# Performance work log

Measured on AMD Instinct MI355X. Metric: run time of the kernel, lower is better.

Reference implementation:

```python
import jax, jax.numpy as jnp
import numpy as np

B, N, D = 8, 4096, 3

def setup_inputs() -> dict:
    key = jax.random.key(0)
    k1, k2 = jax.random.split(key)
    prediction = jax.random.normal(k1, (B, N, D), dtype=jnp.float32)
    ground_truth = jax.random.normal(k2, (B, N, D), dtype=jnp.float32)
    return {"prediction": prediction, "ground_truth": ground_truth}

def reference(prediction, ground_truth):
    batch_size, num, _ = prediction.shape
    # T[b, i, j] = ||pred[b, i] - gt[b, j]||^2  -> [B, N, N]
    diff = prediction[:, :, None, :] - ground_truth[:, None, :, :]
    T = jnp.sum(diff * diff, axis=-1)
    # squeeze() in torch is a no-op for B > 1
    cd_loss = jnp.sum(jnp.min(T, axis=1)) + jnp.sum(jnp.min(T, axis=2))
    return cd_loss / batch_size
```

## Files before the change

### kernel.cpp

```cpp
#include <hip/hip_runtime.h>

#define TPB 256
#define IPT 8
#define NIB 2
#define NPTS 4096
#define NB 8

typedef float v2f __attribute__((ext_vector_type(2)));

static __device__ __forceinline__ v2f pk_fma(v2f a, v2f b, v2f c) {
  v2f d;
  asm("v_pk_fma_f32 %0, %1, %2, %3" : "=v"(d) : "v"(a), "v"(b), "v"(c));
  return d;
}

__global__ __launch_bounds__(TPB, 4) void cd_partial_kernel(
    const float* __restrict__ pred, const float* __restrict__ gt,
    float* __restrict__ partial, float* __restrict__ out, int njb, int jchunk) {
  extern __shared__ float4 spr[];

  if (blockIdx.x == 0 && threadIdx.x == 0) *out = 0.0f;

  int bid = blockIdx.x;
  int jb  = bid % njb;  bid /= njb;
  int ib  = bid & (NIB - 1); bid /= NIB;
  int b   = bid & (NB - 1);  bid /= NB;
  int dir = bid;

  const float* src = (dir == 0) ? pred : gt;
  const float* tgt = (dir == 0) ? gt : pred;
  src += (size_t)b * NPTS * 3;
  tgt += (size_t)b * NPTS * 3;

  const int t = threadIdx.x;

  for (int j = t; j < jchunk; j += TPB) {
    int jj = jb * jchunk + j;
    float gx = tgt[jj * 3 + 0];
    float gy = tgt[jj * 3 + 1];
    float gz = tgt[jj * 3 + 2];
    float gw = fmaf(gx, gx, fmaf(gy, gy, gz * gz));
    int p = j >> 1, h = j & 1;
    float* base = (float*)&spr[2 * p];
    base[0 + h] = gx;
    base[2 + h] = gy;
    base[4 + h] = gz;
    base[6 + h] = gw;
  }

  const int ibase = ib * (TPB * IPT);
  const float4* sv = (const float4*)(src + (size_t)(ibase + t * IPT) * 3);
  float4 A = sv[0], B2 = sv[1], C = sv[2], D = sv[3], E = sv[4], F = sv[5];
  float x[IPT], y[IPT], z[IPT];
  x[0]=A.x;  y[0]=A.y;  z[0]=A.z;
  x[1]=A.w;  y[1]=B2.x; z[1]=B2.y;
  x[2]=B2.z; y[2]=B2.w; z[2]=C.x;
  x[3]=C.y;  y[3]=C.z;  z[3]=C.w;
  x[4]=D.x;  y[4]=D.y;  z[4]=D.z;
  x[5]=D.w;  y[5]=E.x;  z[5]=E.y;
  x[6]=E.z;  y[6]=E.w;  z[6]=F.x;
  x[7]=F.y;  y[7]=F.z;  z[7]=F.w;

  v2f qx2[IPT], qy2[IPT], qz2[IPT];
  float pp[IPT], mn[IPT];
#pragma unroll
  for (int k = 0; k < IPT; ++k) {
    float qx = -2.0f * x[k], qy = -2.0f * y[k], qz = -2.0f * z[k];
    qx2[k] = (v2f){qx, qx};
    qy2[k] = (v2f){qy, qy};
    qz2[k] = (v2f){qz, qz};
    pp[k] = fmaf(x[k], x[k], fmaf(y[k], y[k], z[k] * z[k]));
    mn[k] = 3.4e38f;
  }
  __syncthreads();

  const int npair = jchunk >> 1;
#pragma unroll 8
  for (int p = 0; p < npair; ++p) {
    float4 u = spr[2 * p];
    float4 w = spr[2 * p + 1];
    v2f X = (v2f){u.x, u.y};
    v2f Y = (v2f){u.z, u.w};
    v2f Z = (v2f){w.x, w.y};
    v2f W = (v2f){w.z, w.w};
#pragma unroll
    for (int k = 0; k < IPT; ++k) {
      v2f acc = pk_fma(qz2[k], Z, W);
      acc = pk_fma(qy2[k], Y, acc);
      acc = pk_fma(qx2[k], X, acc);
      mn[k] = fminf(mn[k], fminf(acc.x, acc.y));
    }
  }

  float* outp = partial + ((size_t)((dir * NB + b) * njb + jb)) * NPTS + ibase + t * IPT;
  float4 s0 = make_float4(mn[0] + pp[0], mn[1] + pp[1], mn[2] + pp[2], mn[3] + pp[3]);
  float4 s1 = make_float4(mn[4] + pp[4], mn[5] + pp[5], mn[6] + pp[6], mn[7] + pp[7]);
  ((float4*)outp)[0] = s0;
  ((float4*)outp)[1] = s1;
}

__global__ __launch_bounds__(TPB) void cd_reduce_kernel(
    const float* __restrict__ partial, float* __restrict__ out, int njb) {
  const int total = 2 * NB * NPTS;
  int tid = blockIdx.x * TPB + threadIdx.x;
  float local = 0.0f;
  for (int s = tid; s < total; s += gridDim.x * TPB) {
    int db = s >> 12;
    int i  = s & (NPTS - 1);
    const float* p = partial + (size_t)db * njb * NPTS + i;
    float m = p[0];
#pragma unroll 8
    for (int jb = 1; jb < njb; ++jb) m = fminf(m, p[(size_t)jb * NPTS]);
    local += m;
  }
#pragma unroll
  for (int off = 32; off > 0; off >>= 1) local += __shfl_down(local, off, 64);
  __shared__ float red[TPB / 64];
  int wave = threadIdx.x >> 6;
  int lane = threadIdx.x & 63;
  if (lane == 0) red[wave] = local;
  __syncthreads();
  if (threadIdx.x == 0) {
    float s = 0.0f;
    for (int w = 0; w < TPB / 64; ++w) s += red[w];
    atomicAdd(out, s * (1.0f / NB));
  }
}

extern "C" void kernel_launch(void* const* d_in, const int* in_sizes, int n_in,
                              void* d_out, int out_size, void* d_ws, size_t ws_size,
                              hipStream_t stream) {
  const float* pred = (const float*)d_in[0];
  const float* gt   = (const float*)d_in[1];
  float* out        = (float*)d_out;
  float* partial    = (float*)d_ws;

  int njb = 32;
  {
    size_t per_jb = (size_t)2 * NB * NPTS * sizeof(float);
    size_t need = per_jb * njb;
    if (ws_size < need) {
      njb = (int)(ws_size / per_jb);
      if (njb < 1) njb = 1;
      while (njb & (njb - 1)) njb &= njb - 1;
      if (njb > 32) njb = 32;
    }
  }
  int jchunk = NPTS / njb;

  dim3 grid(2 * NB * NIB * njb);
  size_t lds = (size_t)jchunk * sizeof(float4);
  cd_partial_kernel<<<grid, TPB, lds, stream>>>(pred, gt, partial, out, njb, jchunk);
  cd_reduce_kernel<<<256, TPB, 0, stream>>>(partial, out, njb);
}
```

Before: 39.49 us.

## Use smaller blocks with finer j-split, min3 instruction, and vectorized reduce

Reworks the work split so each partial-min block has 128 threads, covers a quarter of the i range and a 64-point j chunk. This gives 4096 blocks and better load balance. The source-point loads are hoisted before the LDS staging to overlap latency. The inner loop uses v_min3_f32, and the reduce kernel reads float4s with compile-time NJB. In exchange it doubles the partial workspace and drops the runtime fallback for a small workspace, so it risks overflow if the workspace is too small.

```diff
diff --git a/kernel.cpp b/kernel.cpp
--- a/kernel.cpp
+++ b/kernel.cpp
@@ -1,10 +1,12 @@
 #include <hip/hip_runtime.h>
 
-#define TPB 256
+#define TPB 128
 #define IPT 8
-#define NIB 2
+#define NIB 4
 #define NPTS 4096
 #define NB 8
+#define NJB 64
+#define JCH (NPTS / NJB)
 
 typedef float v2f __attribute__((ext_vector_type(2)));
 
@@ -13,18 +15,23 @@
   asm("v_pk_fma_f32 %0, %1, %2, %3" : "=v"(d) : "v"(a), "v"(b), "v"(c));
   return d;
 }
+static __device__ __forceinline__ float min3f(float a, float b, float c) {
+  float d;
+  asm("v_min3_f32 %0, %1, %2, %3" : "=v"(d) : "v"(a), "v"(b), "v"(c));
+  return d;
+}
 
-__global__ __launch_bounds__(TPB, 4) void cd_partial_kernel(
+__global__ __launch_bounds__(TPB, 5) void cd_partial_kernel(
     const float* __restrict__ pred, const float* __restrict__ gt,
-    float* __restrict__ partial, float* __restrict__ out, int njb, int jchunk) {
-  extern __shared__ float4 spr[];
+    float* __restrict__ partial, float* __restrict__ out) {
+  __shared__ float4 spr[JCH];
 
   if (blockIdx.x == 0 && threadIdx.x == 0) *out = 0.0f;
 
   int bid = blockIdx.x;
-  int jb  = bid % njb;  bid /= njb;
-  int ib  = bid & (NIB - 1); bid /= NIB;
-  int b   = bid & (NB - 1);  bid /= NB;
+  int jb  = bid & (NJB - 1); bid >>= 6;
+  int ib  = bid & (NIB - 1); bid >>= 2;
+  int b   = bid & (NB - 1);  bid >>= 3;
   int dir = bid;
 
   const float* src = (dir == 0) ? pred : gt;
@@ -33,14 +40,18 @@
   tgt += (size_t)b * NPTS * 3;
 
   const int t = threadIdx.x;
+  const int ibase = ib * (TPB * IPT);
 
-  for (int j = t; j < jchunk; j += TPB) {
-    int jj = jb * jchunk + j;
+  const float4* sv = (const float4*)(src + (size_t)(ibase + t * IPT) * 3);
+  float4 A = sv[0], B2 = sv[1], C = sv[2], D = sv[3], E = sv[4], F = sv[5];
+
+  if (t < JCH) {
+    int jj = jb * JCH + t;
     float gx = tgt[jj * 3 + 0];
     float gy = tgt[jj * 3 + 1];
     float gz = tgt[jj * 3 + 2];
     float gw = fmaf(gx, gx, fmaf(gy, gy, gz * gz));
-    int p = j >> 1, h = j & 1;
+    int p = t >> 1, h = t & 1;
     float* base = (float*)&spr[2 * p];
     base[0 + h] = gx;
     base[2 + h] = gy;
@@ -48,9 +59,6 @@
     base[6 + h] = gw;
   }
 
-  const int ibase = ib * (TPB * IPT);
-  const float4* sv = (const float4*)(src + (size_t)(ibase + t * IPT) * 3);
-  float4 A = sv[0], B2 = sv[1], C = sv[2], D = sv[3], E = sv[4], F = sv[5];
   float x[IPT], y[IPT], z[IPT];
   x[0]=A.x;  y[0]=A.y;  z[0]=A.z;
   x[1]=A.w;  y[1]=B2.x; z[1]=B2.y;
@@ -74,9 +82,8 @@
   }
   __syncthreads();
 
-  const int npair = jchunk >> 1;
-#pragma unroll 8
-  for (int p = 0; p < npair; ++p) {
+#pragma unroll 4
+  for (int p = 0; p < JCH / 2; ++p) {
     float4 u = spr[2 * p];
     float4 w = spr[2 * p + 1];
     v2f X = (v2f){u.x, u.y};
@@ -88,41 +95,47 @@
       v2f acc = pk_fma(qz2[k], Z, W);
       acc = pk_fma(qy2[k], Y, acc);
       acc = pk_fma(qx2[k], X, acc);
-      mn[k] = fminf(mn[k], fminf(acc.x, acc.y));
+      mn[k] = min3f(mn[k], acc.x, acc.y);
     }
   }
 
-  float* outp = partial + ((size_t)((dir * NB + b) * njb + jb)) * NPTS + ibase + t * IPT;
+  float* outp = partial + ((size_t)((dir * NB + b) * NJB + jb)) * NPTS + ibase + t * IPT;
   float4 s0 = make_float4(mn[0] + pp[0], mn[1] + pp[1], mn[2] + pp[2], mn[3] + pp[3]);
   float4 s1 = make_float4(mn[4] + pp[4], mn[5] + pp[5], mn[6] + pp[6], mn[7] + pp[7]);
   ((float4*)outp)[0] = s0;
   ((float4*)outp)[1] = s1;
 }
 
-__global__ __launch_bounds__(TPB) void cd_reduce_kernel(
-    const float* __restrict__ partial, float* __restrict__ out, int njb) {
-  const int total = 2 * NB * NPTS;
-  int tid = blockIdx.x * TPB + threadIdx.x;
+__global__ __launch_bounds__(256) void cd_reduce_kernel(
+    const float* __restrict__ partial, float* __restrict__ out) {
+  const int quads = 2 * NB * NPTS / 4;
+  int tid = blockIdx.x * 256 + threadIdx.x;
   float local = 0.0f;
-  for (int s = tid; s < total; s += gridDim.x * TPB) {
-    int db = s >> 12;
-    int i  = s & (NPTS - 1);
-    const float* p = partial + (size_t)db * njb * NPTS + i;
-    float m = p[0];
-#pragma unroll 8
-    for (int jb = 1; jb < njb; ++jb) m = fminf(m, p[(size_t)jb * NPTS]);
-    local += m;
+  for (int q = tid; q < quads; q += gridDim.x * 256) {
+    int db = q >> 10;
+    int i4 = (q & 1023) * 4;
+    const float4* p = (const float4*)(partial + (size_t)db * NJB * NPTS + i4);
+    float4 m = p[0];
+#pragma unroll
+    for (int jb = 1; jb < NJB; ++jb) {
+      float4 v = p[(size_t)jb * (NPTS / 4)];
+      m.x = fminf(m.x, v.x);
+      m.y = fminf(m.y, v.y);
+      m.z = fminf(m.z, v.z);
+      m.w = fminf(m.w, v.w);
+    }
+    local += (m.x + m.y) + (m.z + m.w);
   }
 #pragma unroll
   for (int off = 32; off > 0; off >>= 1) local += __shfl_down(local, off, 64);
-  __shared__ float red[TPB / 64];
+  __shared__ float red[256 / 64];
   int wave = threadIdx.x >> 6;
   int lane = threadIdx.x & 63;
   if (lane == 0) red[wave] = local;
   __syncthreads();
   if (threadIdx.x == 0) {
     float s = 0.0f;
-    for (int w = 0; w < TPB / 64; ++w) s += red[w];
+    for (int w = 0; w < 256 / 64; ++w) s += red[w];
     atomicAdd(out, s * (1.0f / NB));
   }
 }
@@ -135,21 +148,7 @@
   float* out        = (float*)d_out;
   float* partial    = (float*)d_ws;
 
-  int njb = 32;
-  {
-    size_t per_jb = (size_t)2 * NB * NPTS * sizeof(float);
-    size_t need = per_jb * njb;
-    if (ws_size < need) {
-      njb = (int)(ws_size / per_jb);
-      if (njb < 1) njb = 1;
-      while (njb & (njb - 1)) njb &= njb - 1;
-      if (njb > 32) njb = 32;
-    }
-  }
-  int jchunk = NPTS / njb;
-
-  dim3 grid(2 * NB * NIB * njb);
-  size_t lds = (size_t)jchunk * sizeof(float4);
-  cd_partial_kernel<<<grid, TPB, lds, stream>>>(pred, gt, partial, out, njb, jchunk);
-  cd_reduce_kernel<<<256, TPB, 0, stream>>>(partial, out, njb);
+  dim3 grid(2 * NB * NIB * NJB);
+  cd_partial_kernel<<<grid, TPB, 0, stream>>>(pred, gt, partial, out);
+  cd_reduce_kernel<<<64, 256, 0, stream>>>(partial, out);
 }
```

After: 41.18 us. +4.3%, slower.
